# Performance work log

Hardware: AMD Instinct MI355X
Metric: run time of the kernel (lower is better)

## Reference

```python
import jax, jax.numpy as jnp
import numpy as np

N_QUBITS = 4
DIM = 16
N_QLAYERS = 2

def _cnot_perm(c, t):
    idx = np.arange(DIM)
    cbit = (idx >> (N_QUBITS - 1 - c)) & 1
    return np.where(cbit == 1, idx ^ (1 << (N_QUBITS - 1 - t)), idx)

# ring entanglement: CNOT(0,1), CNOT(1,2), CNOT(2,3), CNOT(3,0)
RING_PERMS = [jnp.asarray(_cnot_perm(i, (i + 1) % N_QUBITS)) for i in range(N_QUBITS)]
_idx = np.arange(DIM)
ZSIGNS = jnp.asarray(np.stack([1.0 - 2.0 * ((_idx >> (N_QUBITS - 1 - q)) & 1) for q in range(N_QUBITS)], axis=1).astype(np.float32))  # (16, 4)

def _rx(t):
    c = jnp.cos(t / 2).astype(jnp.complex64)
    s = jnp.sin(t / 2).astype(jnp.complex64)
    return jnp.stack([jnp.stack([c, -1j * s]), jnp.stack([-1j * s, c])])

def _ry(t):
    c = jnp.cos(t / 2).astype(jnp.complex64)
    s = jnp.sin(t / 2).astype(jnp.complex64)
    return jnp.stack([jnp.stack([c, -s]), jnp.stack([s, c])])

def _rz(t):
    e = jnp.exp(-0.5j * t.astype(jnp.complex64))
    z = jnp.zeros((), jnp.complex64)
    return jnp.stack([jnp.stack([e, z]), jnp.stack([z, jnp.conj(e)])])

def _apply_1q(state, g, q):
    # wire 0 is the most significant bit (PennyLane convention)
    s = state.reshape(2 ** q, 2, 2 ** (N_QUBITS - 1 - q))
    return jnp.einsum('ij,ajc->aic', g, s).reshape(DIM)

def _circuit(angles, qw):
    # angles: (4,), qw: (n_qlayers, 4, 3); returns PauliZ expvals (4,)
    state = jnp.zeros(DIM, jnp.complex64).at[0].set(1.0)
    for q in range(N_QUBITS):
        state = _apply_1q(state, _ry(angles[q]), q)
    for l in range(N_QLAYERS):
        for q in range(N_QUBITS):
            state = _apply_1q(state, _rx(qw[l, q, 0]), q)
            state = _apply_1q(state, _ry(qw[l, q, 1]), q)
            state = _apply_1q(state, _rz(qw[l, q, 2]), q)
        for p in RING_PERMS:
            state = state[p]
    probs = jnp.abs(state) ** 2
    return probs @ ZSIGNS

def _conv(x, w, b, stride, pad):
    y = jax.lax.conv_general_dilated(x, w, (stride, stride), [(pad, pad), (pad, pad)], dimension_numbers=('NCHW', 'OIHW', 'NCHW'))
    return y + b[None, :, None, None]

def _bn(x, g, b, m, v):
    scale = (g / jnp.sqrt(v + 1e-5))[None, :, None, None]
    return (x - m[None, :, None, None]) * scale + b[None, :, None, None]

def _forward(x, c1w, c1b, bn1g, bn1b, bn1m, bn1v, c2w, c2b, bn2g, bn2b, bn2m, bn2v, c3w, c3b, bn3g, bn3b, bn3m, bn3v, pre_w, pre_b, qw, pw1, pb1, pw2, pb2):
    B = x.shape[0]
    h = jax.nn.relu(_bn(_conv(x, c1w, c1b, 4, 3), bn1g, bn1b, bn1m, bn1v))   # (B,32,56,56)
    h = jax.nn.relu(_bn(_conv(h, c2w, c2b, 2, 1), bn2g, bn2b, bn2m, bn2v))   # (B,64,28,28)
    h = jax.nn.relu(_bn(_conv(h, c3w, c3b, 2, 1), bn3g, bn3b, bn3m, bn3v))   # (B,128,14,14)
    h = h.reshape(B, 128, 2, 7, 2, 7).mean(axis=(3, 5))                       # AdaptiveAvgPool2d((2,2))
    f = h.reshape(B, 128 * 4)
    ang = jnp.tanh(f @ pre_w.T + pre_b) * jnp.pi                              # (B,4)
    qout = jax.vmap(lambda a: _circuit(a, qw))(ang)                            # (B,4) batched statevector sim
    h1 = jax.nn.relu(qout @ pw1.T + pb1)                                       # dropout inactive (eval)
    return h1 @ pw2.T + pb2

def setup_inputs() -> dict:
    key = jax.random.key(0)
    ks = jax.random.split(key, 16)
    d = {
        'x': jax.random.normal(ks[0], (128, 3, 224, 224), jnp.float32),
        'c1w': jax.random.normal(ks[1], (32, 3, 7, 7), jnp.float32) * 0.05,
        'c1b': jax.random.normal(ks[2], (32,), jnp.float32) * 0.05,
        'bn1g': jnp.ones((32,), jnp.float32), 'bn1b': jnp.zeros((32,), jnp.float32),
        'bn1m': jnp.zeros((32,), jnp.float32), 'bn1v': jnp.ones((32,), jnp.float32),
        'c2w': jax.random.normal(ks[3], (64, 32, 3, 3), jnp.float32) * 0.05,
        'c2b': jax.random.normal(ks[4], (64,), jnp.float32) * 0.05,
        'bn2g': jnp.ones((64,), jnp.float32), 'bn2b': jnp.zeros((64,), jnp.float32),
        'bn2m': jnp.zeros((64,), jnp.float32), 'bn2v': jnp.ones((64,), jnp.float32),
        'c3w': jax.random.normal(ks[5], (128, 64, 3, 3), jnp.float32) * 0.05,
        'c3b': jax.random.normal(ks[6], (128,), jnp.float32) * 0.05,
        'bn3g': jnp.ones((128,), jnp.float32), 'bn3b': jnp.zeros((128,), jnp.float32),
        'bn3m': jnp.zeros((128,), jnp.float32), 'bn3v': jnp.ones((128,), jnp.float32),
        'pre_w': jax.random.normal(ks[7], (4, 512), jnp.float32) * 0.04,
        'pre_b': jax.random.normal(ks[8], (4,), jnp.float32) * 0.04,
        'qw': jax.random.normal(ks[9], (2, 4, 3), jnp.float32) * 0.1,
        'pw1': jax.random.normal(ks[10], (64, 4), jnp.float32) * 0.5,
        'pb1': jax.random.normal(ks[11], (64,), jnp.float32) * 0.5,
        'pw2': jax.random.normal(ks[12], (5, 64), jnp.float32) * 0.12,
        'pb2': jax.random.normal(ks[13], (5,), jnp.float32) * 0.12,
    }
    return d

def reference(x, c1w, c1b, bn1g, bn1b, bn1m, bn1v, c2w, c2b, bn2g, bn2b, bn2m, bn2v, c3w, c3b, bn3g, bn3b, bn3m, bn3v, pre_w, pre_b, qw, pw1, pb1, pw2, pb2):
    return _forward(x, c1w, c1b, bn1g, bn1b, bn1m, bn1v, c2w, c2b, bn2g, bn2b, bn2m, bn2v, c3w, c3b, bn3g, bn3b, bn3m, bn3v, pre_w, pre_b, qw, pw1, pb1, pw2, pb2)
```

## Files before the change

### kernel.cpp

```cpp
#include <hip/hip_runtime.h>
#include <math.h>

#define DEV __device__ __forceinline__

typedef __attribute__((ext_vector_type(8))) __bf16 bf16x8;
typedef __attribute__((ext_vector_type(4))) float f32x4;

__global__ void prep_weights(
    const float* __restrict__ c1w, const float* __restrict__ c1b,
    const float* __restrict__ g1, const float* __restrict__ b1,
    const float* __restrict__ m1, const float* __restrict__ v1,
    const float* __restrict__ c2w, const float* __restrict__ c2b,
    const float* __restrict__ g2, const float* __restrict__ b2,
    const float* __restrict__ m2, const float* __restrict__ v2,
    const float* __restrict__ c3w, const float* __restrict__ c3b,
    const float* __restrict__ g3, const float* __restrict__ b3,
    const float* __restrict__ m3, const float* __restrict__ v3,
    __bf16* __restrict__ wb1, __bf16* __restrict__ wb2, __bf16* __restrict__ wb3,
    float* __restrict__ sc1, float* __restrict__ sh1,
    float* __restrict__ sc2, float* __restrict__ sh2,
    float* __restrict__ sc3, float* __restrict__ sh3)
{
    int gid = blockIdx.x * 256 + threadIdx.x;
    int gs = gridDim.x * 256;
    for (int e = gid; e < 32 * 192; e += gs) {
        int oc = e / 192, k = e % 192, rr = k >> 3, kw = k & 7;
        wb1[e] = (rr < 21 && kw >= 1) ? (__bf16)c1w[oc * 147 + rr * 7 + kw - 1]
                                      : (__bf16)0.f;
    }
    for (int e = gid; e < 64 * 384; e += gs) {
        int oc = e / 384, k = e % 384, rr = k >> 2, kw = k & 3;
        wb2[e] = (kw >= 1) ? (__bf16)c2w[oc * 288 + rr * 3 + kw - 1] : (__bf16)0.f;
    }
    for (int e = gid; e < 128 * 768; e += gs) {
        int oc = e / 768, k = e % 768, rr = k >> 2, kw = k & 3;
        wb3[e] = (kw >= 1) ? (__bf16)c3w[oc * 576 + rr * 3 + kw - 1] : (__bf16)0.f;
    }
    if (gid < 32) {
        float s = g1[gid] * rsqrtf(v1[gid] + 1e-5f);
        sc1[gid] = s; sh1[gid] = (c1b[gid] - m1[gid]) * s + b1[gid];
    } else if (gid < 96) {
        int i = gid - 32;
        float s = g2[i] * rsqrtf(v2[i] + 1e-5f);
        sc2[i] = s; sh2[i] = (c2b[i] - m2[i]) * s + b2[i];
    } else if (gid < 224) {
        int i = gid - 96;
        float s = g3[i] * rsqrtf(v3[i] + 1e-5f);
        sc3[i] = s; sh3[i] = (c3b[i] - m3[i]) * s + b3[i];
    }
}

__global__ __launch_bounds__(256, 3) void conv1_kernel(
    const float* __restrict__ x,
    const __bf16* __restrict__ wb,
    const float* __restrict__ scale, const float* __restrict__ shift,
    __bf16* __restrict__ out)
{
    constexpr int IHW = 224 * 224, OHW = 56 * 56, LDR = 72;
    __shared__ __attribute__((aligned(16))) __bf16 Is[256 * LDR];
    __shared__ __attribute__((aligned(16))) __bf16 Ws[32 * LDR];

    const int tid = threadIdx.x;
    const int sb0 = blockIdx.x * 256;
    const int sm = tid;

    int a_n, a_ih0, a_iw0;
    {
        int m = sb0 + sm;
        a_n = m / OHW;
        int rem = m % OHW;
        a_ih0 = (rem / 56) * 4 - 3;
        a_iw0 = (rem % 56) * 4 - 3;
    }
    unsigned ihok = 0;
    #pragma unroll
    for (int t = 0; t < 7; ++t)
        ihok |= (unsigned)(((a_ih0 + t) >= 0) && ((a_ih0 + t) < 224)) << t;
    const bool left = (a_iw0 < 0);
    const int boff = a_n * 3 * IHW + a_ih0 * 224 + (a_iw0 - 1);

    const int w_oc = tid >> 3, w_j = tid & 7;
    const int wave = tid >> 6, lane = tid & 63;
    const int quad = lane >> 4, l16 = lane & 15;

    f32x4 acc[2][4] = {};

    #pragma unroll
    for (int ci = 0; ci < 3; ++ci) {
        const int k0 = ci * 64;
        bf16x8 hv[8];
        #pragma unroll
        for (int r = 0; r < 8; ++r) {
            const int rr = ci * 8 + r;
            if (rr >= 21) {
                hv[r] = (bf16x8){};
            } else {
                const int ic = rr / 7, kh = rr % 7;
                int off = boff + (ic * IHW + kh * 224);
                int o0 = off < 0 ? 0 : off;
                int o1 = (off + 4) < 0 ? 0 : (off + 4);
                float4 A = *(const float4*)(x + o0);
                float4 B = *(const float4*)(x + o1);
                float va[8] = {A.x, A.y, A.z, A.w, B.x, B.y, B.z, B.w};
                bool rok = (ihok >> kh) & 1u;
                #pragma unroll
                for (int j = 0; j < 8; ++j) va[j] = rok ? va[j] : 0.f;
                #pragma unroll
                for (int j = 1; j <= 3; ++j) va[j] = left ? 0.f : va[j];
                bf16x8 h;
                #pragma unroll
                for (int j = 0; j < 8; ++j) h[j] = (__bf16)va[j];
                hv[r] = h;
            }
        }
        bf16x8 wv = *(const bf16x8*)&wb[(size_t)w_oc * 192 + k0 + w_j * 8];

        __syncthreads();
        #pragma unroll
        for (int r = 0; r < 8; ++r)
            *(bf16x8*)&Is[sm * LDR + r * 8] = hv[r];
        *(bf16x8*)&Ws[w_oc * LDR + w_j * 8] = wv;
        __syncthreads();

        #pragma unroll
        for (int kk = 0; kk < 2; ++kk) {
            bf16x8 afr[2], bfr[4];
            #pragma unroll
            for (int mt = 0; mt < 2; ++mt)
                afr[mt] = *(const bf16x8*)&Ws[(mt * 16 + l16) * LDR + kk * 32 + quad * 8];
            #pragma unroll
            for (int nt = 0; nt < 4; ++nt)
                bfr[nt] = *(const bf16x8*)&Is[(wave * 64 + nt * 16 + l16) * LDR + kk * 32 + quad * 8];
            #pragma unroll
            for (int mt = 0; mt < 2; ++mt)
                #pragma unroll
                for (int nt = 0; nt < 4; ++nt)
                    acc[mt][nt] = __builtin_amdgcn_mfma_f32_16x16x32_bf16(
                        afr[mt], bfr[nt], acc[mt][nt], 0, 0, 0);
        }
    }

    #pragma unroll
    for (int mt = 0; mt < 2; ++mt) {
        #pragma unroll
        for (int r = 0; r < 4; ++r) {
            int oc = mt * 16 + quad * 4 + r;
            float scl = scale[oc], shf = shift[oc];
            #pragma unroll
            for (int nt = 0; nt < 4; ++nt) {
                int sg = sb0 + wave * 64 + nt * 16 + l16;
                int n = sg / OHW, s = sg % OHW;
                float v = fmaf(acc[mt][nt][r], scl, shf);
                v = v > 0.f ? v : 0.f;
                out[((size_t)n * 32 + oc) * OHW + s] = (__bf16)v;
            }
        }
    }
}

template<int NOCT, int IC, int IH, int IW, int OH, int OW, int OC,
         int KTP, int KCH, int GXS>
DEV void conv_body64(
    const __bf16* __restrict__ xo,
    const __bf16* __restrict__ wb,
    const float* __restrict__ scale, const float* __restrict__ shift,
    __bf16* __restrict__ out, __bf16* Is, __bf16* Ws)
{
    constexpr int KS = 3, S = 2, P = 1;
    constexpr int KITER = KCH / 64;
    constexpr int OHW = OH * OW;
    constexpr int IHW = IH * IW;
    constexpr int LDR = 72;
    constexpr int WLD = NOCT / 2;

    const int tid = threadIdx.x;
    int bx = blockIdx.x;
    if (GXS > 0) bx = (bx & 7) * GXS + (bx >> 3);
    const int sb0 = bx * 256;
    const int oc0 = blockIdx.y * (NOCT * 16);

    const int sm = tid;
    int a_n, a_ih0, a_iw0;
    {
        int m = sb0 + sm;
        a_n = m / OHW;
        int rem = m % OHW;
        a_ih0 = (rem / OW) * S - P;
        a_iw0 = (rem % OW) * S - P;
    }
    unsigned ihok = 0;
    #pragma unroll
    for (int t = 0; t < KS; ++t)
        ihok |= (unsigned)(((a_ih0 + t) >= 0) && ((a_ih0 + t) < IH)) << t;
    const bool left = (a_iw0 < 0);
    const __bf16* xp = xo + ((size_t)a_n * IC * IHW + (ptrdiff_t)a_ih0 * IW
                             + (a_iw0 - 1));

    const int wave = tid >> 6, lane = tid & 63;
    const int quad = lane >> 4, l16 = lane & 15;

    f32x4 acc[NOCT][4] = {};

    #pragma unroll
    for (int ci = 0; ci < KITER; ++ci) {
        const int k0 = ci * 64;

        union { unsigned u[32]; bf16x8 v[8]; } Pk;
        #pragma unroll
        for (int r = 0; r < 16; ++r) {
            const int rr = (k0 / 4) + r;
            const int ic = rr / KS, kh = rr % KS;
            const unsigned* rp = (const unsigned*)(xp + (ic * IHW + kh * IW));
            unsigned t0 = rp[0], t1 = rp[1];
            bool rok = (ihok >> kh) & 1u;
            t0 = rok ? t0 : 0u;
            t1 = rok ? t1 : 0u;
            t0 = left ? (t0 & 0x0000FFFFu) : t0;
            Pk.u[r * 2]     = t0;
            Pk.u[r * 2 + 1] = t1;
        }
        bf16x8 wv[WLD];
        #pragma unroll
        for (int i = 0; i < WLD; ++i) {
            int e = i * 256 + tid;
            wv[i] = *(const bf16x8*)&wb[(size_t)(oc0 + (e >> 3)) * KTP + k0 + (e & 7) * 8];
        }

        __syncthreads();
        #pragma unroll
        for (int q = 0; q < 8; ++q)
            *(bf16x8*)&Is[sm * LDR + q * 8] = Pk.v[q];
        #pragma unroll
        for (int i = 0; i < WLD; ++i) {
            int e = i * 256 + tid;
            *(bf16x8*)&Ws[(e >> 3) * LDR + (e & 7) * 8] = wv[i];
        }
        __syncthreads();

        #pragma unroll
        for (int kk = 0; kk < 2; ++kk) {
            bf16x8 afr[NOCT], bfr[4];
            #pragma unroll
            for (int mt = 0; mt < NOCT; ++mt)
                afr[mt] = *(const bf16x8*)&Ws[(mt * 16 + l16) * LDR + kk * 32 + quad * 8];
            #pragma unroll
            for (int nt = 0; nt < 4; ++nt)
                bfr[nt] = *(const bf16x8*)&Is[(wave * 64 + nt * 16 + l16) * LDR + kk * 32 + quad * 8];
            #pragma unroll
            for (int mt = 0; mt < NOCT; ++mt)
                #pragma unroll
                for (int nt = 0; nt < 4; ++nt)
                    acc[mt][nt] = __builtin_amdgcn_mfma_f32_16x16x32_bf16(
                        afr[mt], bfr[nt], acc[mt][nt], 0, 0, 0);
        }
    }

    #pragma unroll
    for (int mt = 0; mt < NOCT; ++mt) {
        #pragma unroll
        for (int r = 0; r < 4; ++r) {
            int oc = oc0 + mt * 16 + quad * 4 + r;
            float scl = scale[oc], shf = shift[oc];
            #pragma unroll
            for (int nt = 0; nt < 4; ++nt) {
                int sg = sb0 + wave * 64 + nt * 16 + l16;
                int n = sg / OHW, s = sg % OHW;
                float v = fmaf(acc[mt][nt][r], scl, shf);
                v = v > 0.f ? v : 0.f;
                out[((size_t)n * OC + oc) * OHW + s] = (__bf16)v;
            }
        }
    }
}

__global__ __launch_bounds__(256, 3) void conv2_kernel(
    const __bf16* __restrict__ xo, const __bf16* __restrict__ wb,
    const float* __restrict__ scale, const float* __restrict__ shift,
    __bf16* __restrict__ out)
{
    __shared__ __attribute__((aligned(16))) __bf16 Is[256 * 72];
    __shared__ __attribute__((aligned(16))) __bf16 Ws[64 * 72];
    conv_body64<4, 32, 56, 56, 28, 28, 64, 384, 384, 49>(
        xo, wb, scale, shift, out, Is, Ws);
}

__global__ __launch_bounds__(256, 3) void conv3_kernel(
    const __bf16* __restrict__ xo, const __bf16* __restrict__ wb,
    const float* __restrict__ scale, const float* __restrict__ shift,
    __bf16* __restrict__ out)
{
    __shared__ __attribute__((aligned(16))) __bf16 Is[256 * 72];
    __shared__ __attribute__((aligned(16))) __bf16 Ws[32 * 72];
    conv_body64<2, 64, 28, 28, 14, 14, 128, 768, 768, 0>(
        xo, wb, scale, shift, out, Is, Ws);
}

__global__ __launch_bounds__(256) void head_kernel(
    const __bf16* __restrict__ c3o,
    const float* __restrict__ pre_w, const float* __restrict__ pre_b,
    const float* __restrict__ qw,
    const float* __restrict__ pw1, const float* __restrict__ pb1,
    const float* __restrict__ pw2, const float* __restrict__ pb2,
    float* __restrict__ out)
{
    __shared__ __attribute__((aligned(16))) __bf16 slab[128 * 196];
    __shared__ float f[512];
    __shared__ float ang[4];
    __shared__ float zexp[4];
    __shared__ float h1[64];

    int b = blockIdx.x;
    int t = threadIdx.x;

    {
        const bf16x8* src = (const bf16x8*)(c3o + (size_t)b * 128 * 196);
        bf16x8* dst = (bf16x8*)slab;
        #pragma unroll
        for (int i = 0; i < 13; ++i) {
            int e = t + i * 256;
            if (e < 3136) dst[e] = src[e];
        }
    }
    __syncthreads();

    for (int p = t; p < 512; p += 256) {
        int c = p >> 2, i = (p >> 1) & 1, j = p & 1;
        int base = c * 196 + (i * 7) * 14 + j * 7;
        float s = 0.f;
        #pragma unroll
        for (int u = 0; u < 7; ++u)
            #pragma unroll
            for (int v = 0; v < 7; ++v)
                s += (float)slab[base + u * 14 + v];
        f[p] = s * (1.f / 49.f);
    }
    __syncthreads();

    int wv = t >> 6, lane = t & 63;
    float partial = 0.f;
    for (int d = lane; d < 512; d += 64)
        partial += f[d] * pre_w[wv * 512 + d];
    #pragma unroll
    for (int off = 32; off > 0; off >>= 1)
        partial += __shfl_down(partial, off, 64);
    if (lane == 0)
        ang[wv] = tanhf(partial + pre_b[wv]) * 3.14159265358979323846f;
    __syncthreads();

    if (t < 16) {
        const int i = t;
        float re = (i == 0) ? 1.f : 0.f;
        float im = 0.f;

        #pragma unroll
        for (int q = 0; q < 4; ++q) {
            const int m = 8 >> q;
            float th = ang[q] * 0.5f;
            float c = cosf(th), s = sinf(th);
            float pr = __shfl_xor(re, m, 64);
            float pi = __shfl_xor(im, m, 64);
            float ts = (i & m) ? s : -s;
            re = c * re + ts * pr;
            im = c * im + ts * pi;
        }
        #pragma unroll
        for (int l = 0; l < 2; ++l) {
            #pragma unroll
            for (int q = 0; q < 4; ++q) {
                const int m = 8 >> q;
                const float* qq = qw + (l * 4 + q) * 3;
                {
                    float th = qq[0] * 0.5f;
                    float c = cosf(th), s = sinf(th);
                    float pr = __shfl_xor(re, m, 64);
                    float pi = __shfl_xor(im, m, 64);
                    float rn = c * re + s * pi;
                    im = c * im - s * pr;
                    re = rn;
                }
                {
                    float th = qq[1] * 0.5f;
                    float c = cosf(th), s = sinf(th);
                    float pr = __shfl_xor(re, m, 64);
                    float pi = __shfl_xor(im, m, 64);
                    float ts = (i & m) ? s : -s;
                    re = c * re + ts * pr;
                    im = c * im + ts * pi;
                }
                {
                    float th = qq[2] * 0.5f;
                    float c = cosf(th), s = sinf(th);
                    float ts = (i & m) ? s : -s;
                    float rn = c * re - ts * im;
                    im = c * im + ts * re;
                    re = rn;
                }
            }
            #pragma unroll
            for (int e = 0; e < 4; ++e) {
                const int cm = 8 >> e, tm = 8 >> ((e + 1) & 3);
                float pr = __shfl_xor(re, tm, 64);
                float pi = __shfl_xor(im, tm, 64);
                bool sw = (i & cm) != 0;
                re = sw ? pr : re;
                im = sw ? pi : im;
            }
        }
        float p2 = re * re + im * im;
        #pragma unroll
        for (int q = 0; q < 4; ++q) {
            const int m = 8 >> q;
            float v = (i & m) ? -p2 : p2;
            v += __shfl_xor(v, 1, 64);
            v += __shfl_xor(v, 2, 64);
            v += __shfl_xor(v, 4, 64);
            v += __shfl_xor(v, 8, 64);
            if (i == 0) zexp[q] = v;
        }
    }
    __syncthreads();

    if (t < 64) {
        float s = pb1[t];
        #pragma unroll
        for (int k = 0; k < 4; ++k) s += zexp[k] * pw1[t * 4 + k];
        h1[t] = s > 0.f ? s : 0.f;
    }
    __syncthreads();

    if (t < 5) {
        float s = pb2[t];
        for (int k = 0; k < 64; ++k) s += h1[k] * pw2[t * 64 + k];
        out[b * 5 + t] = s;
    }
}

extern "C" void kernel_launch(void* const* d_in, const int* in_sizes, int n_in,
                              void* d_out, int out_size, void* d_ws, size_t ws_size,
                              hipStream_t stream) {
    const float* x    = (const float*)d_in[0];
    const float* c1w  = (const float*)d_in[1];
    const float* c1b  = (const float*)d_in[2];
    const float* bn1g = (const float*)d_in[3];
    const float* bn1b = (const float*)d_in[4];
    const float* bn1m = (const float*)d_in[5];
    const float* bn1v = (const float*)d_in[6];
    const float* c2w  = (const float*)d_in[7];
    const float* c2b  = (const float*)d_in[8];
    const float* bn2g = (const float*)d_in[9];
    const float* bn2b = (const float*)d_in[10];
    const float* bn2m = (const float*)d_in[11];
    const float* bn2v = (const float*)d_in[12];
    const float* c3w  = (const float*)d_in[13];
    const float* c3bi = (const float*)d_in[14];
    const float* bn3g = (const float*)d_in[15];
    const float* bn3b = (const float*)d_in[16];
    const float* bn3m = (const float*)d_in[17];
    const float* bn3v = (const float*)d_in[18];
    const float* prw  = (const float*)d_in[19];
    const float* prb  = (const float*)d_in[20];
    const float* qw   = (const float*)d_in[21];
    const float* pw1  = (const float*)d_in[22];
    const float* pb1  = (const float*)d_in[23];
    const float* pw2  = (const float*)d_in[24];
    const float* pb2  = (const float*)d_in[25];

    const int N = in_sizes[0] / (3 * 224 * 224);
    const size_t NC1 = (size_t)N * 32 * 56 * 56;
    const size_t NC2 = (size_t)N * 64 * 28 * 28;
    const size_t NC3 = (size_t)N * 128 * 14 * 14;

    __bf16* ws_h = (__bf16*)d_ws;
    __bf16* c1o = ws_h + 64;
    __bf16* c2o = ws_h + 64 + NC1 + 64 + 64;
    __bf16* c3o = ws_h + 64 + NC1 + 64 + 64 + NC2 + 64;
    __bf16* wb1 = c3o + NC3;
    __bf16* wb2 = wb1 + 32 * 192;
    __bf16* wb3 = wb2 + 64 * 384;
    float* sc1 = (float*)(wb3 + 128 * 768);
    float* sh1 = sc1 + 32;
    float* sc2 = sh1 + 32;  float* sh2 = sc2 + 64;
    float* sc3 = sh2 + 64;  float* sh3 = sc3 + 128;

    prep_weights<<<192, 256, 0, stream>>>(
        c1w, c1b, bn1g, bn1b, bn1m, bn1v,
        c2w, c2b, bn2g, bn2b, bn2m, bn2v,
        c3w, c3bi, bn3g, bn3b, bn3m, bn3v,
        wb1, wb2, wb3, sc1, sh1, sc2, sh2, sc3, sh3);

    conv1_kernel<<<dim3(401408 / 256, 1), 256, 0, stream>>>(x, wb1, sc1, sh1, c1o);
    conv2_kernel<<<dim3(100352 / 256, 1), 256, 0, stream>>>(c1o, wb2, sc2, sh2, c2o);
    conv3_kernel<<<dim3(25088 / 256, 4), 256, 0, stream>>>(c2o, wb3, sc3, sh3, c3o);
    head_kernel<<<N, 256, 0, stream>>>(c3o, prw, prb, qw,
                                       pw1, pb1, pw2, pb2, (float*)d_out);
}
```

Measured before the change: 229.7 us.

## Software-pipeline global loads of next K-chunk behind MFMA compute in conv kernels

Both conv kernels now issue the global loads for the next K iteration into registers right after writing the current chunk to LDS, so the loads overlap the MFMA work. The full __syncthreads are replaced by raw s_barrier calls plus an explicit lgkmcnt wait. Masking and bf16 conversion move to after the loads arrive. This raises register pressure, and the hand-placed barrier and waitcnt are fragile if vmcnt ordering is not handled by the compiler.

```diff
diff --git a/kernel.cpp b/kernel.cpp
--- a/kernel.cpp
+++ b/kernel.cpp
@@ -85,42 +85,54 @@
 
     f32x4 acc[2][4] = {};
 
-    #pragma unroll
-    for (int ci = 0; ci < 3; ++ci) {
-        const int k0 = ci * 64;
-        bf16x8 hv[8];
+    float4 RA[8], RB[8];
+    bf16x8 wv;
+
+    auto LOADI = [&](int ci) {
         #pragma unroll
         for (int r = 0; r < 8; ++r) {
             const int rr = ci * 8 + r;
-            if (rr >= 21) {
-                hv[r] = (bf16x8){};
-            } else {
+            if (rr < 21) {
                 const int ic = rr / 7, kh = rr % 7;
                 int off = boff + (ic * IHW + kh * 224);
                 int o0 = off < 0 ? 0 : off;
                 int o1 = (off + 4) < 0 ? 0 : (off + 4);
-                float4 A = *(const float4*)(x + o0);
-                float4 B = *(const float4*)(x + o1);
-                float va[8] = {A.x, A.y, A.z, A.w, B.x, B.y, B.z, B.w};
+                RA[r] = *(const float4*)(x + o0);
+                RB[r] = *(const float4*)(x + o1);
+            }
+        }
+        wv = *(const bf16x8*)&wb[(size_t)w_oc * 192 + ci * 64 + w_j * 8];
+    };
+
+    LOADI(0);
+
+    #pragma unroll
+    for (int ci = 0; ci < 3; ++ci) {
+        __builtin_amdgcn_s_barrier();
+        #pragma unroll
+        for (int r = 0; r < 8; ++r) {
+            const int rr = ci * 8 + r;
+            bf16x8 h;
+            if (rr >= 21) {
+                h = (bf16x8){};
+            } else {
+                const int kh = rr % 7;
+                float va[8] = {RA[r].x, RA[r].y, RA[r].z, RA[r].w,
+                               RB[r].x, RB[r].y, RB[r].z, RB[r].w};
                 bool rok = (ihok >> kh) & 1u;
                 #pragma unroll
                 for (int j = 0; j < 8; ++j) va[j] = rok ? va[j] : 0.f;
                 #pragma unroll
                 for (int j = 1; j <= 3; ++j) va[j] = left ? 0.f : va[j];
-                bf16x8 h;
                 #pragma unroll
                 for (int j = 0; j < 8; ++j) h[j] = (__bf16)va[j];
-                hv[r] = h;
-            }
-        }
-        bf16x8 wv = *(const bf16x8*)&wb[(size_t)w_oc * 192 + k0 + w_j * 8];
-
-        __syncthreads();
-        #pragma unroll
-        for (int r = 0; r < 8; ++r)
-            *(bf16x8*)&Is[sm * LDR + r * 8] = hv[r];
+            }
+            *(bf16x8*)&Is[sm * LDR + r * 8] = h;
+        }
         *(bf16x8*)&Ws[w_oc * LDR + w_j * 8] = wv;
-        __syncthreads();
+        if (ci + 1 < 3) LOADI(ci + 1);
+        asm volatile("s_waitcnt lgkmcnt(0)" ::: "memory");
+        __builtin_amdgcn_s_barrier();
 
         #pragma unroll
         for (int kk = 0; kk < 2; ++kk) {
@@ -201,41 +213,56 @@
 
     f32x4 acc[NOCT][4] = {};
 
-    #pragma unroll
-    for (int ci = 0; ci < KITER; ++ci) {
+    unsigned Pu[32];
+    bf16x8 wv[WLD];
+
+    auto LOADI = [&](int ci) {
         const int k0 = ci * 64;
-
-        union { unsigned u[32]; bf16x8 v[8]; } Pk;
         #pragma unroll
         for (int r = 0; r < 16; ++r) {
             const int rr = (k0 / 4) + r;
             const int ic = rr / KS, kh = rr % KS;
             const unsigned* rp = (const unsigned*)(xp + (ic * IHW + kh * IW));
-            unsigned t0 = rp[0], t1 = rp[1];
-            bool rok = (ihok >> kh) & 1u;
-            t0 = rok ? t0 : 0u;
-            t1 = rok ? t1 : 0u;
-            t0 = left ? (t0 & 0x0000FFFFu) : t0;
-            Pk.u[r * 2]     = t0;
-            Pk.u[r * 2 + 1] = t1;
-        }
-        bf16x8 wv[WLD];
+            Pu[r * 2]     = rp[0];
+            Pu[r * 2 + 1] = rp[1];
+        }
         #pragma unroll
         for (int i = 0; i < WLD; ++i) {
             int e = i * 256 + tid;
             wv[i] = *(const bf16x8*)&wb[(size_t)(oc0 + (e >> 3)) * KTP + k0 + (e & 7) * 8];
         }
-
-        __syncthreads();
-        #pragma unroll
-        for (int q = 0; q < 8; ++q)
-            *(bf16x8*)&Is[sm * LDR + q * 8] = Pk.v[q];
+    };
+
+    LOADI(0);
+
+    #pragma unroll
+    for (int ci = 0; ci < KITER; ++ci) {
+        __builtin_amdgcn_s_barrier();
+        #pragma unroll
+        for (int q = 0; q < 8; ++q) {
+            union { unsigned u[4]; bf16x8 v; } tm;
+            #pragma unroll
+            for (int h = 0; h < 2; ++h) {
+                const int r = 2 * q + h;
+                const int kh = (ci * 16 + r) % KS;
+                unsigned t0 = Pu[r * 2], t1 = Pu[r * 2 + 1];
+                bool rok = (ihok >> kh) & 1u;
+                t0 = rok ? t0 : 0u;
+                t1 = rok ? t1 : 0u;
+                t0 = left ? (t0 & 0x0000FFFFu) : t0;
+                tm.u[h * 2]     = t0;
+                tm.u[h * 2 + 1] = t1;
+            }
+            *(bf16x8*)&Is[sm * LDR + q * 8] = tm.v;
+        }
         #pragma unroll
         for (int i = 0; i < WLD; ++i) {
             int e = i * 256 + tid;
             *(bf16x8*)&Ws[(e >> 3) * LDR + (e & 7) * 8] = wv[i];
         }
-        __syncthreads();
+        if (ci + 1 < KITER) LOADI(ci + 1);
+        asm volatile("s_waitcnt lgkmcnt(0)" ::: "memory");
+        __builtin_amdgcn_s_barrier();
 
         #pragma unroll
         for (int kk = 0; kk < 2; ++kk) {
```

Result: no change. 231.6 us (+0.8%).
